# Kernel optimization log

Hardware: AMD Instinct MI355X
Metric: run time of the kernel (lower is better)

The kernel has to match this reference:

```python
import jax, jax.numpy as jnp
import numpy as np

B, N = 2, 384
NODE_DIM, NODE_HIDDEN, EDGE_DIM = 128, 256, 64
EDGE_H1 = 2 * EDGE_DIM + 2 * NODE_DIM  # 384, forced by concat in edge update
EDGE_H2 = 128
HEADS = 8
SCALE = 1.0 / float(np.sqrt(NODE_HIDDEN // HEADS))  # torch uses node_hidden//heads
EPS = 1e-5


def _w(k, out_dim, in_dim):
    return jax.random.normal(k, (out_dim, in_dim), dtype=jnp.float32) * 0.02


def setup_inputs() -> dict:
    ks = jax.random.split(jax.random.key(0), 32)
    inp = {
        'x': jax.random.normal(ks[0], (B, N, NODE_DIM), dtype=jnp.float32),
        'dense_adj': jax.random.normal(ks[1], (B, N, N, EDGE_DIM), dtype=jnp.float32),
        'wnq': _w(ks[2], NODE_DIM, NODE_DIM),
        'wnk': _w(ks[3], NODE_DIM, NODE_DIM),
        'wnv': _w(ks[4], NODE_DIM, NODE_DIM),
        'weq': _w(ks[5], NODE_DIM, EDGE_DIM),
        'wek': _w(ks[6], NODE_DIM, EDGE_DIM),
        'wev': _w(ks[7], NODE_DIM, EDGE_DIM),
        'nfc1_w': _w(ks[8], NODE_DIM, NODE_DIM),
        'nfc1_b': jnp.zeros((NODE_DIM,), jnp.float32),
        'ln1_g': jnp.ones((NODE_DIM,), jnp.float32),
        'ln1_b': jnp.zeros((NODE_DIM,), jnp.float32),
        'nfc2_w': _w(ks[9], NODE_HIDDEN, NODE_DIM),
        'nfc2_b': jnp.zeros((NODE_HIDDEN,), jnp.float32),
        'nfc3_w': _w(ks[10], NODE_DIM, NODE_HIDDEN),
        'nfc3_b': jnp.zeros((NODE_DIM,), jnp.float32),
        'ln2_g': jnp.ones((NODE_DIM,), jnp.float32),
        'ln2_b': jnp.zeros((NODE_DIM,), jnp.float32),
        'efc1_w': _w(ks[11], EDGE_DIM, EDGE_H1),
        'efc1_b': jnp.zeros((EDGE_DIM,), jnp.float32),
        'efc2_w': _w(ks[12], EDGE_DIM, EDGE_DIM),
        'efc2_b': jnp.zeros((EDGE_DIM,), jnp.float32),
        'eln1_g': jnp.ones((EDGE_DIM,), jnp.float32),
        'eln1_b': jnp.zeros((EDGE_DIM,), jnp.float32),
        'efc3_w': _w(ks[13], EDGE_H2, EDGE_DIM),
        'efc3_b': jnp.zeros((EDGE_H2,), jnp.float32),
        'efc4_w': _w(ks[14], EDGE_DIM, EDGE_H2),
        'efc4_b': jnp.zeros((EDGE_DIM,), jnp.float32),
        'eln2_g': jnp.ones((EDGE_DIM,), jnp.float32),
        'eln2_b': jnp.zeros((EDGE_DIM,), jnp.float32),
    }
    return inp


def layer_norm(t, g, b):
    m = jnp.mean(t, axis=-1, keepdims=True)
    v = jnp.mean((t - m) ** 2, axis=-1, keepdims=True)
    return (t - m) * jax.lax.rsqrt(v + EPS) * g + b


def rt_attention(x, adj, wnq, wnk, wnv, weq, wek, wev):
    Bb, Nn, D = x.shape
    d = D // HEADS
    def sn(t):  # [B,N,D] -> [B,H,N,d]
        return t.reshape(Bb, Nn, HEADS, d).transpose(0, 2, 1, 3)
    def se(t):  # [B,N,N,D] -> [B,H,N,N,d]
        return t.reshape(Bb, Nn, Nn, HEADS, d).transpose(0, 3, 1, 2, 4)
    # edge-augmented per-pair q,k,v: [B,H,i,j,d]
    q = sn(x @ wnq.T)[:, :, :, None, :] + se(adj @ weq.T)
    k = sn(x @ wnk.T)[:, :, None, :, :] + se(adj @ wek.T)
    v = sn(x @ wnv.T)[:, :, None, :, :] + se(adj @ wev.T)
    scores = jnp.sum(q * k, axis=-1) * SCALE          # [B,H,i,j]
    attn = jax.nn.softmax(scores, axis=-1)            # softmax over keys j
    out = jnp.einsum('bhij,bhijc->bhic', attn, v)     # [B,H,N,d]
    # torch reshape_from_batches interleaves as [B,N,d,H] -> [B,N,d*H]
    return out.transpose(0, 2, 3, 1).reshape(Bb, Nn, D)


def reference(x, dense_adj, wnq, wnk, wnv, weq, wek, wev,
              nfc1_w, nfc1_b, ln1_g, ln1_b, nfc2_w, nfc2_b, nfc3_w, nfc3_b,
              ln2_g, ln2_b, efc1_w, efc1_b, efc2_w, efc2_b, eln1_g, eln1_b,
              efc3_w, efc3_b, efc4_w, efc4_b, eln2_g, eln2_b):
    attn_out = rt_attention(x, dense_adj, wnq, wnk, wnv, weq, wek, wev)
    res = attn_out @ nfc1_w.T + nfc1_b
    x = layer_norm(x + res, ln1_g, ln1_b)
    res = jax.nn.relu(x @ nfc2_w.T + nfc2_b) @ nfc3_w.T + nfc3_b
    x = layer_norm(x + res, ln2_g, ln2_b)
    # edge update: [adj_ij, adj_ji, x_j (source), x_i (target)]
    Bb, Nn, D = x.shape
    src = jnp.broadcast_to(x[:, None, :, :], (Bb, Nn, Nn, D))
    tgt = jnp.broadcast_to(x[:, :, None, :], (Bb, Nn, Nn, D))
    rev = jnp.swapaxes(dense_adj, -2, -3)
    ua = jnp.concatenate([dense_adj, rev, src, tgt], axis=-1)  # [B,N,N,EDGE_H1]
    res = jax.nn.relu(ua @ efc1_w.T + efc1_b) @ efc2_w.T + efc2_b
    adj = layer_norm(dense_adj + res, eln1_g, eln1_b)
    res = jax.nn.relu(adj @ efc3_w.T + efc3_b) @ efc4_w.T + efc4_b
    adj = layer_norm(adj + res, eln2_g, eln2_b)
    return (x, adj)
```

## Files before the change

### kernel.cpp

```cpp
#include <hip/hip_runtime.h>
#include <hip/hip_bf16.h>

typedef unsigned short u16;
typedef unsigned int u32;

#define NB 2
#define NN 384
#define ND 128
#define NE 64
#define NHD 8
#define NHID 256
#define EH1 384
#define EH2 128
#define LN_EPS 1e-5f
#define ATT_SCALE 0.17677669529663687f

#define XOUT_ELEMS (NB * NN * ND)
#define ADJ_ELEMS ((size_t)NB * NN * NN * NE)
#define OUT_ELEMS (XOUT_ELEMS + ADJ_ELEMS)
#define SCRATCH_F32 (4 * XOUT_ELEMS)

typedef __attribute__((ext_vector_type(4))) float f32x4;
typedef __attribute__((ext_vector_type(8))) short s16x8;
#define MFMA16(a, b, c) __builtin_amdgcn_mfma_f32_16x16x32_bf16(a, b, c, 0, 0, 0)

__device__ __forceinline__ float bflo(u32 u) {
  return __builtin_bit_cast(float, u << 16);
}
__device__ __forceinline__ float bfhi(u32 u) {
  return __builtin_bit_cast(float, u & 0xffff0000u);
}
__device__ __forceinline__ u16 bfr(float f) {
  return __builtin_bit_cast(u16, __float2bfloat16(f));
}
__device__ __forceinline__ float bfu(u16 h) {
  return __builtin_bit_cast(float, ((u32)h) << 16);
}
__device__ __forceinline__ u32 packbf(float a, float b) {
  return (u32)bfr(a) | ((u32)bfr(b) << 16);
}
__device__ __forceinline__ float wsum64(float v) {
#pragma unroll
  for (int o = 32; o > 0; o >>= 1) v += __shfl_xor(v, o, 64);
  return v;
}
__device__ __forceinline__ float wmax64(float v) {
#pragma unroll
  for (int o = 32; o > 0; o >>= 1) v = fmaxf(v, __shfl_xor(v, o, 64));
  return v;
}

__device__ __forceinline__ s16x8 cvt_frag(const float* p) {
  float4 a = *(const float4*)p;
  float4 c = *(const float4*)(p + 4);
  s16x8 r;
  r[0] = (short)bfr(a.x); r[1] = (short)bfr(a.y);
  r[2] = (short)bfr(a.z); r[3] = (short)bfr(a.w);
  r[4] = (short)bfr(c.x); r[5] = (short)bfr(c.y);
  r[6] = (short)bfr(c.z); r[7] = (short)bfr(c.w);
  return r;
}

__device__ __forceinline__ void cvt8_hl(const float* p, uint4& hi, uint4& lo) {
  float4 a = *(const float4*)p;
  float4 c = *(const float4*)(p + 4);
  float v[8] = {a.x, a.y, a.z, a.w, c.x, c.y, c.z, c.w};
  u32 hw[4], lw[4];
#pragma unroll
  for (int e = 0; e < 4; ++e) {
    u16 h0 = bfr(v[2 * e]), h1 = bfr(v[2 * e + 1]);
    u16 l0 = bfr(v[2 * e] - bfu(h0));
    u16 l1 = bfr(v[2 * e + 1] - bfu(h1));
    hw[e] = (u32)h0 | ((u32)h1 << 16);
    lw[e] = (u32)l0 | ((u32)l1 << 16);
  }
  hi.x = hw[0]; hi.y = hw[1]; hi.z = hw[2]; hi.w = hw[3];
  lo.x = lw[0]; lo.y = lw[1]; lo.z = lw[2]; lo.w = lw[3];
}

__global__ void k_node_qkv(const float* __restrict__ x,
                           const float* __restrict__ wq,
                           const float* __restrict__ wk,
                           const float* __restrict__ wv,
                           float* __restrict__ nq, float* __restrict__ nk,
                           float* __restrict__ nv) {
  int row = blockIdx.x;
  int t = threadIdx.x;
  __shared__ float xs[ND];
  xs[t] = x[row * ND + t];
  __syncthreads();
  float aq = 0.f, ak = 0.f, av = 0.f;
  for (int k = 0; k < ND; ++k) {
    float xv = xs[k];
    aq += xv * wq[t * ND + k];
    ak += xv * wk[t * ND + k];
    av += xv * wv[t * ND + k];
  }
  nq[row * ND + t] = aq;
  nk[row * ND + t] = ak;
  nv[row * ND + t] = av;
}

#define ATJ 128
struct AttnS {
  u16 Ahi[ATJ][NE];
  u16 Alo[ATJ][NE];
  float sc[NHD][NN];
  float psum[NHD][NE];
  float part[4][ND];
};

__global__ void __launch_bounds__(512) k_attn(
    const float* __restrict__ adj,
    const float* __restrict__ weq,
    const float* __restrict__ wek,
    const float* __restrict__ wev,
    const float* __restrict__ nq,
    const float* __restrict__ nk,
    const float* __restrict__ nv,
    float* __restrict__ att) {
  __shared__ AttnS s;
  int bi = blockIdx.x;
  int b = bi / NN;
  int t = threadIdx.x;
  int h = t >> 6;
  int l = t & 63;
  int lr = l & 15, lk = l >> 4;

  s16x8 BQ[2], BK[2];
  {
    const float* wqp = weq + (size_t)(h * 16 + lr) * NE + lk * 8;
    const float* wkp = wek + (size_t)(h * 16 + lr) * NE + lk * 8;
    BQ[0] = cvt_frag(wqp); BQ[1] = cvt_frag(wqp + 32);
    BK[0] = cvt_frag(wkp); BK[1] = cvt_frag(wkp + 32);
  }
  float nqd = nq[(size_t)bi * ND + h * 16 + lr];

  for (int tile = 0; tile < NN / ATJ; ++tile) {
    int jbase = tile * ATJ;
    __syncthreads();
    for (int p = t; p < ATJ * 8; p += 512) {
      int row = p >> 3, u = p & 7;
      const float* src = adj + ((size_t)bi * NN + jbase + row) * NE + u * 8;
      uint4 hi, lo;
      cvt8_hl(src, hi, lo);
      int byt = (row * 128 + u * 16) ^ ((row & 7) << 4);
      *(uint4*)((char*)s.Ahi + byt) = hi;
      *(uint4*)((char*)s.Alo + byt) = lo;
    }
    __syncthreads();

#pragma unroll
    for (int sub = 0; sub < ATJ / 16; ++sub) {
      int trow = sub * 16 + lr;
      int swz = (trow & 7) << 4;
      f32x4 eq = {0.f, 0.f, 0.f, 0.f}, ek = {0.f, 0.f, 0.f, 0.f};
#pragma unroll
      for (int ks = 0; ks < 2; ++ks) {
        int byt = (trow * 128 + ks * 64 + lk * 16) ^ swz;
        s16x8 ah = *(const s16x8*)((const char*)s.Ahi + byt);
        s16x8 al = *(const s16x8*)((const char*)s.Alo + byt);
        eq = MFMA16(ah, BQ[ks], eq);
        eq = MFMA16(al, BQ[ks], eq);
        ek = MFMA16(ah, BK[ks], ek);
        ek = MFMA16(al, BK[ks], ek);
      }
#pragma unroll
      for (int r = 0; r < 4; ++r) {
        int j = jbase + sub * 16 + lk * 4 + r;
        float kv = nk[((size_t)b * NN + j) * ND + h * 16 + lr] + ek[r];
        float prod = (nqd + eq[r]) * kv;
#pragma unroll
        for (int o = 8; o > 0; o >>= 1) prod += __shfl_xor(prod, o, 64);
        if (lr == 0) s.sc[h][j] = prod * ATT_SCALE;
      }
    }
  }
  __syncthreads();

  {
    float vals[NN / 64];
    float m = -1e30f;
#pragma unroll
    for (int r = 0; r < NN / 64; ++r) {
      vals[r] = s.sc[h][l + 64 * r];
      m = fmaxf(m, vals[r]);
    }
    m = wmax64(m);
    float sum = 0.f;
#pragma unroll
    for (int r = 0; r < NN / 64; ++r) {
      vals[r] = __expf(vals[r] - m);
      sum += vals[r];
    }
    sum = wsum64(sum);
    float rinv = 1.f / sum;
#pragma unroll
    for (int r = 0; r < NN / 64; ++r) s.sc[h][l + 64 * r] = vals[r] * rinv;
  }

  {
    float pacc = 0.f;
    const float* ab = adj + (size_t)bi * NN * NE + l;
    const float* prow = s.sc[h];
#pragma unroll 4
    for (int j = 0; j < NN; ++j) pacc += prow[j] * ab[(size_t)j * NE];
    s.psum[h][l] = pacc;
  }
  __syncthreads();

  {
    int c = t & 127, grp = t >> 7;
    int hc = c >> 4;
    float acc = 0.f;
    const float* nvb = nv + (size_t)b * NN * ND + c;
    const float* pr = s.sc[hc];
#pragma unroll 4
    for (int j = grp * (NN / 4); j < (grp + 1) * (NN / 4); ++j)
      acc += pr[j] * nvb[(size_t)j * ND];
    s.part[grp][c] = acc;
  }
  __syncthreads();
  if (t < ND) {
    int c = t, hc = c >> 4;
    float acc = s.part[0][c] + s.part[1][c] + s.part[2][c] + s.part[3][c];
    const float4* wr = (const float4*)(wev + c * NE);
    const float* ps = s.psum[hc];
#pragma unroll
    for (int k4 = 0; k4 < NE / 4; ++k4) {
      float4 w4 = wr[k4];
      acc += w4.x * ps[4 * k4] + w4.y * ps[4 * k4 + 1] +
             w4.z * ps[4 * k4 + 2] + w4.w * ps[4 * k4 + 3];
    }
    att[(size_t)bi * ND + (c & 15) * NHD + hc] = acc;
  }
}

struct FfnS {
  float atts[ND];
  float tvb[ND];
  float x1[ND];
  float hb[NHID];
  float stats[2];
};

__global__ void k_node_ffn(const float* __restrict__ x,
                           const float* __restrict__ att,
                           const float* __restrict__ w1, const float* __restrict__ b1,
                           const float* __restrict__ g1, const float* __restrict__ bb1,
                           const float* __restrict__ w2, const float* __restrict__ b2,
                           const float* __restrict__ w3, const float* __restrict__ b3,
                           const float* __restrict__ g2, const float* __restrict__ bb2,
                           float* __restrict__ xout) {
  __shared__ FfnS s;
  int row = blockIdx.x;
  int tid = threadIdx.x;
  if (tid < ND) s.atts[tid] = att[row * ND + tid];
  __syncthreads();

  if (tid < ND) {
    float acc = b1[tid];
    for (int k = 0; k < ND; ++k) acc += s.atts[k] * w1[tid * ND + k];
    s.tvb[tid] = x[row * ND + tid] + acc;
  }
  __syncthreads();
  if (tid < 64) {
    float v0 = s.tvb[tid], v1 = s.tvb[tid + 64];
    float m = wsum64(v0 + v1) * (1.f / ND);
    float d0 = v0 - m, d1 = v1 - m;
    float var = wsum64(d0 * d0 + d1 * d1) * (1.f / ND);
    if (tid == 0) {
      s.stats[0] = m;
      s.stats[1] = rsqrtf(var + LN_EPS);
    }
  }
  __syncthreads();
  if (tid < ND)
    s.x1[tid] = (s.tvb[tid] - s.stats[0]) * s.stats[1] * g1[tid] + bb1[tid];
  __syncthreads();

  {
    float acc = b2[tid];
    for (int k = 0; k < ND; ++k) acc += s.x1[k] * w2[tid * ND + k];
    s.hb[tid] = fmaxf(acc, 0.f);
  }
  __syncthreads();

  if (tid < ND) {
    float acc = b3[tid];
    for (int k = 0; k < NHID; ++k) acc += s.hb[k] * w3[tid * NHID + k];
    s.tvb[tid] = s.x1[tid] + acc;
  }
  __syncthreads();
  if (tid < 64) {
    float v0 = s.tvb[tid], v1 = s.tvb[tid + 64];
    float m = wsum64(v0 + v1) * (1.f / ND);
    float d0 = v0 - m, d1 = v1 - m;
    float var = wsum64(d0 * d0 + d1 * d1) * (1.f / ND);
    if (tid == 0) {
      s.stats[0] = m;
      s.stats[1] = rsqrtf(var + LN_EPS);
    }
  }
  __syncthreads();
  if (tid < ND) {
    float o = (s.tvb[tid] - s.stats[0]) * s.stats[1] * g2[tid] + bb2[tid];
    xout[row * ND + tid] = o;
  }
}

#define EMT 32

struct E1M {
  u16 Ahi[EMT][256];
  u16 Alo[EMT][256];
  u16 Hhi[EMT][NE];
  u16 Hlo[EMT][NE];
};

__global__ void __launch_bounds__(512) k_edge1(
    const float* __restrict__ adj, const float* __restrict__ xq,
    const float* __restrict__ w1, const float* __restrict__ b1,
    const float* __restrict__ w2, const float* __restrict__ b2,
    const float* __restrict__ g, const float* __restrict__ bb,
    float* __restrict__ adj1out) {
  __shared__ E1M s;
  int bi = blockIdx.x;
  int b = bi / NN, i = bi % NN;
  int t = threadIdx.x;
  int w = t >> 6, l = t & 63;
  int m16 = (w & 1) * 16;
  int n16 = (w >> 1) * 16;
  int lr = l & 15, lk = l >> 4;

  s16x8 B1[8], B2[2];
  {
    const float* wr = w1 + (size_t)(n16 + lr) * EH1 + lk * 8;
#pragma unroll
    for (int ks = 0; ks < 8; ++ks) B1[ks] = cvt_frag(wr + ks * 32);
    const float* w2r = w2 + (size_t)(n16 + lr) * NE + lk * 8;
#pragma unroll
    for (int ks = 0; ks < 2; ++ks) B2[ks] = cvt_frag(w2r + ks * 32);
  }
  float bias1;
  {
    float ci = 0.f;
    const float* xr = xq + (size_t)bi * ND;
    const float* wr = w1 + (size_t)(n16 + lr) * EH1 + 256;
#pragma unroll 4
    for (int k = 0; k < ND; ++k) ci += xr[k] * bfu(bfr(wr[k]));
    bias1 = b1[n16 + lr] + ci;
  }
  float bias2 = b2[n16 + lr];
  float gl = g[l], bl = bb[l];

  for (int mt = 0; mt < NN / EMT; ++mt) {
    int jbase = mt * EMT;
    __syncthreads();
    for (int p = t; p < EMT * 32; p += 512) {
      int row = p >> 5, uu = p & 31;
      const float* src;
      if (uu < 8)
        src = adj + ((size_t)bi * NN + jbase + row) * NE + uu * 8;
      else if (uu < 16)
        src = adj + ((size_t)(b * NN + jbase + row) * NN + i) * NE + (uu - 8) * 8;
      else
        src = xq + (size_t)(b * NN + jbase + row) * ND + (uu - 16) * 8;
      uint4 hi, lo;
      cvt8_hl(src, hi, lo);
      int byt = (row * 512 + uu * 16) ^ ((row & 7) << 4);
      *(uint4*)((char*)s.Ahi + byt) = hi;
      *(uint4*)((char*)s.Alo + byt) = lo;
    }
    __syncthreads();

    f32x4 acc = {0.f, 0.f, 0.f, 0.f};
    int arow = m16 + lr;
    int aswz = (arow & 7) << 4;
#pragma unroll
    for (int ks = 0; ks < 8; ++ks) {
      int byt = (arow * 512 + ks * 64 + lk * 16) ^ aswz;
      s16x8 ah = *(const s16x8*)((const char*)s.Ahi + byt);
      s16x8 al = *(const s16x8*)((const char*)s.Alo + byt);
      acc = MFMA16(ah, B1[ks], acc);
      acc = MFMA16(al, B1[ks], acc);
    }
#pragma unroll
    for (int r = 0; r < 4; ++r) {
      float hv = fmaxf(acc[r] + bias1, 0.f);
      u16 hh = bfr(hv);
      u16 hl = bfr(hv - bfu(hh));
      int row = m16 + lk * 4 + r;
      int byt = (row * 128 + (n16 + lr) * 2) ^ ((row & 7) << 4);
      *(u16*)((char*)s.Hhi + byt) = hh;
      *(u16*)((char*)s.Hlo + byt) = hl;
    }
    __syncthreads();

    f32x4 acc2 = {0.f, 0.f, 0.f, 0.f};
#pragma unroll
    for (int ks = 0; ks < 2; ++ks) {
      int byt = (arow * 128 + ks * 64 + lk * 16) ^ aswz;
      s16x8 ah = *(const s16x8*)((const char*)s.Hhi + byt);
      s16x8 al = *(const s16x8*)((const char*)s.Hlo + byt);
      acc2 = MFMA16(ah, B2[ks], acc2);
      acc2 = MFMA16(al, B2[ks], acc2);
    }
    __syncthreads();
    float* tvb = (float*)s.Hhi;
#pragma unroll
    for (int r = 0; r < 4; ++r) {
      int row = m16 + lk * 4 + r;
      int col = n16 + lr;
      int abyt = (row * 512 + col * 2) ^ ((row & 7) << 4);
      float aorig = bfu(*(const u16*)((const char*)s.Ahi + abyt)) +
                    bfu(*(const u16*)((const char*)s.Alo + abyt));
      tvb[row * NE + col] = aorig + acc2[r] + bias2;
    }
    __syncthreads();
#pragma unroll
    for (int rr = 0; rr < EMT / 8; ++rr) {
      int row = w * (EMT / 8) + rr;
      float tv = tvb[row * NE + l];
      float mean = wsum64(tv) * (1.f / NE);
      float dv = tv - mean;
      float var = wsum64(dv * dv) * (1.f / NE);
      float o = dv * rsqrtf(var + LN_EPS) * gl + bl;
      adj1out[((size_t)bi * NN + jbase + row) * NE + l] = o;
    }
  }
}

struct E2M {
  u16 Ahi[EMT][NE];
  u16 Alo[EMT][NE];
  u16 Hhi[EMT][EH2];
  u16 Hlo[EMT][EH2];
};

__global__ void __launch_bounds__(512) k_edge2(
    float* __restrict__ adjio,
    const float* __restrict__ w3, const float* __restrict__ b3,
    const float* __restrict__ w4, const float* __restrict__ b4,
    const float* __restrict__ g, const float* __restrict__ bb) {
  __shared__ E2M s;
  int bi = blockIdx.x;
  int t = threadIdx.x;
  int w = t >> 6, l = t & 63;
  int m16 = (w & 1) * 16;
  int nb = (w >> 1) * 2;
  int n16 = (w >> 1) * 16;
  int lr = l & 15, lk = l >> 4;

  s16x8 B3[2][2], B4[4];
  {
#pragma unroll
    for (int n = 0; n < 2; ++n) {
      const float* wr = w3 + (size_t)((nb + n) * 16 + lr) * NE + lk * 8;
#pragma unroll
      for (int ks = 0; ks < 2; ++ks) B3[n][ks] = cvt_frag(wr + ks * 32);
    }
    const float* w4r = w4 + (size_t)(n16 + lr) * EH2 + lk * 8;
#pragma unroll
    for (int ks = 0; ks < 4; ++ks) B4[ks] = cvt_frag(w4r + ks * 32);
  }
  float bias3[2] = {b3[nb * 16 + lr], b3[(nb + 1) * 16 + lr]};
  float bias4 = b4[n16 + lr];
  float gl = g[l], bl = bb[l];

  for (int mt = 0; mt < NN / EMT; ++mt) {
    int jbase = mt * EMT;
    __syncthreads();
    for (int p = t; p < EMT * 8; p += 512) {
      int row = p >> 3, u = p & 7;
      const float* src = adjio + ((size_t)bi * NN + jbase + row) * NE + u * 8;
      uint4 hi, lo;
      cvt8_hl(src, hi, lo);
      int byt = (row * 128 + u * 16) ^ ((row & 7) << 4);
      *(uint4*)((char*)s.Ahi + byt) = hi;
      *(uint4*)((char*)s.Alo + byt) = lo;
    }
    __syncthreads();

    f32x4 a3[2] = {{0.f, 0.f, 0.f, 0.f}, {0.f, 0.f, 0.f, 0.f}};
    int arow = m16 + lr;
    int aswz = (arow & 7) << 4;
#pragma unroll
    for (int ks = 0; ks < 2; ++ks) {
      int byt = (arow * 128 + ks * 64 + lk * 16) ^ aswz;
      s16x8 ah = *(const s16x8*)((const char*)s.Ahi + byt);
      s16x8 al = *(const s16x8*)((const char*)s.Alo + byt);
#pragma unroll
      for (int n = 0; n < 2; ++n) {
        a3[n] = MFMA16(ah, B3[n][ks], a3[n]);
        a3[n] = MFMA16(al, B3[n][ks], a3[n]);
      }
    }
#pragma unroll
    for (int n = 0; n < 2; ++n) {
#pragma unroll
      for (int r = 0; r < 4; ++r) {
        float hv = fmaxf(a3[n][r] + bias3[n], 0.f);
        u16 hh = bfr(hv);
        u16 hl = bfr(hv - bfu(hh));
        int row = m16 + lk * 4 + r;
        int byt = (row * 256 + ((nb + n) * 16 + lr) * 2) ^ ((row & 7) << 4);
        *(u16*)((char*)s.Hhi + byt) = hh;
        *(u16*)((char*)s.Hlo + byt) = hl;
      }
    }
    __syncthreads();

    f32x4 a4 = {0.f, 0.f, 0.f, 0.f};
#pragma unroll
    for (int ks = 0; ks < 4; ++ks) {
      int byt = (arow * 256 + ks * 64 + lk * 16) ^ aswz;
      s16x8 ah = *(const s16x8*)((const char*)s.Hhi + byt);
      s16x8 al = *(const s16x8*)((const char*)s.Hlo + byt);
      a4 = MFMA16(ah, B4[ks], a4);
      a4 = MFMA16(al, B4[ks], a4);
    }
    __syncthreads();
    float* tvb = (float*)s.Hhi;
#pragma unroll
    for (int r = 0; r < 4; ++r) {
      int row = m16 + lk * 4 + r;
      int col = n16 + lr;
      int abyt = (row * 128 + col * 2) ^ ((row & 7) << 4);
      float aorig = bfu(*(const u16*)((const char*)s.Ahi + abyt)) +
                    bfu(*(const u16*)((const char*)s.Alo + abyt));
      tvb[row * NE + col] = aorig + a4[r] + bias4;
    }
    __syncthreads();
#pragma unroll
    for (int rr = 0; rr < EMT / 8; ++rr) {
      int row = w * (EMT / 8) + rr;
      float tv = tvb[row * NE + l];
      float mean = wsum64(tv) * (1.f / NE);
      float dv = tv - mean;
      float var = wsum64(dv * dv) * (1.f / NE);
      float o = dv * rsqrtf(var + LN_EPS) * gl + bl;
      adjio[((size_t)bi * NN + jbase + row) * NE + l] = o;
    }
  }
}

extern "C" void kernel_launch(void* const* d_in, const int* in_sizes, int n_in,
                              void* d_out, int out_size, void* d_ws, size_t ws_size,
                              hipStream_t stream) {
  (void)in_sizes; (void)n_in; (void)out_size; (void)d_ws; (void)ws_size;
  const float* x      = (const float*)d_in[0];
  const float* adj    = (const float*)d_in[1];
  const float* wnq    = (const float*)d_in[2];
  const float* wnk    = (const float*)d_in[3];
  const float* wnv    = (const float*)d_in[4];
  const float* weq    = (const float*)d_in[5];
  const float* wek    = (const float*)d_in[6];
  const float* wev    = (const float*)d_in[7];
  const float* nfc1_w = (const float*)d_in[8];
  const float* nfc1_b = (const float*)d_in[9];
  const float* ln1_g  = (const float*)d_in[10];
  const float* ln1_b  = (const float*)d_in[11];
  const float* nfc2_w = (const float*)d_in[12];
  const float* nfc2_b = (const float*)d_in[13];
  const float* nfc3_w = (const float*)d_in[14];
  const float* nfc3_b = (const float*)d_in[15];
  const float* ln2_g  = (const float*)d_in[16];
  const float* ln2_b  = (const float*)d_in[17];
  const float* efc1_w = (const float*)d_in[18];
  const float* efc1_b = (const float*)d_in[19];
  const float* efc2_w = (const float*)d_in[20];
  const float* efc2_b = (const float*)d_in[21];
  const float* eln1_g = (const float*)d_in[22];
  const float* eln1_b = (const float*)d_in[23];
  const float* efc3_w = (const float*)d_in[24];
  const float* efc3_b = (const float*)d_in[25];
  const float* efc4_w = (const float*)d_in[26];
  const float* efc4_b = (const float*)d_in[27];
  const float* eln2_g = (const float*)d_in[28];
  const float* eln2_b = (const float*)d_in[29];

  float* outf = (float*)d_out;
  float* outadj = outf + XOUT_ELEMS;

  float* scratch = outf + OUT_ELEMS - SCRATCH_F32;
  float* nq  = scratch;
  float* nk  = scratch + XOUT_ELEMS;
  float* nv  = scratch + 2 * XOUT_ELEMS;
  float* att = scratch + 3 * XOUT_ELEMS;

  k_node_qkv<<<NB * NN, 128, 0, stream>>>(x, wnq, wnk, wnv, nq, nk, nv);
  k_attn<<<NB * NN, 512, 0, stream>>>(adj, weq, wek, wev, nq, nk, nv, att);
  k_node_ffn<<<NB * NN, 256, 0, stream>>>(x, att, nfc1_w, nfc1_b, ln1_g, ln1_b,
                                          nfc2_w, nfc2_b, nfc3_w, nfc3_b,
                                          ln2_g, ln2_b, outf);
  k_edge1<<<NB * NN, 512, 0, stream>>>(adj, outf, efc1_w, efc1_b, efc2_w, efc2_b,
                                       eln1_g, eln1_b, outadj);
  k_edge2<<<NB * NN, 512, 0, stream>>>(outadj, efc3_w, efc3_b, efc4_w, efc4_b,
                                       eln2_g, eln2_b);
}
```

Measured before the change: 570.3 us.

## Prefetch adj tiles into registers and fuse online softmax with edge-value accumulation

The attention kernel now loads the next adj tile into registers while the current tile is being processed, and preloads nk values for the whole tile into a register array. An online softmax (running max and sum) computes the probability-weighted sum of adj rows from the bf16 hi/lo tile already in shared memory, instead of rereading all of adj from global memory in a second pass. This removes a second pass over global memory and hides load latency, at the cost of more registers, extra shared memory for pe, and a small precision change from reconstructing adj from its hi/lo bf16 split.

```diff
diff --git a/kernel.cpp b/kernel.cpp
--- a/kernel.cpp
+++ b/kernel.cpp
@@ -61,9 +61,7 @@
   return r;
 }
 
-__device__ __forceinline__ void cvt8_hl(const float* p, uint4& hi, uint4& lo) {
-  float4 a = *(const float4*)p;
-  float4 c = *(const float4*)(p + 4);
+__device__ __forceinline__ void cvt8v(float4 a, float4 c, uint4& hi, uint4& lo) {
   float v[8] = {a.x, a.y, a.z, a.w, c.x, c.y, c.z, c.w};
   u32 hw[4], lw[4];
 #pragma unroll
@@ -76,6 +74,10 @@
   }
   hi.x = hw[0]; hi.y = hw[1]; hi.z = hw[2]; hi.w = hw[3];
   lo.x = lw[0]; lo.y = lw[1]; lo.z = lw[2]; lo.w = lw[3];
+}
+
+__device__ __forceinline__ void cvt8_hl(const float* p, uint4& hi, uint4& lo) {
+  cvt8v(*(const float4*)p, *(const float4*)(p + 4), hi, lo);
 }
 
 __global__ void k_node_qkv(const float* __restrict__ x,
@@ -106,6 +108,7 @@
   u16 Ahi[ATJ][NE];
   u16 Alo[ATJ][NE];
   float sc[NHD][NN];
+  float pe[NHD][ATJ];
   float psum[NHD][NE];
   float part[4][ND];
 };
@@ -136,19 +139,52 @@
   }
   float nqd = nq[(size_t)bi * ND + h * 16 + lr];
 
+  int row0 = t >> 3, u0 = t & 7;
+  int row1 = row0 + 64, u1 = u0;
+  float4 pa0, pb0, pa1, pb1;
+  {
+    const float* s0 = adj + ((size_t)bi * NN + row0) * NE + u0 * 8;
+    const float* s1 = adj + ((size_t)bi * NN + row1) * NE + u1 * 8;
+    pa0 = *(const float4*)s0; pb0 = *(const float4*)(s0 + 4);
+    pa1 = *(const float4*)s1; pb1 = *(const float4*)(s1 + 4);
+  }
+
+  float m_run = -1e30f, lsum = 0.f, psacc = 0.f;
+
   for (int tile = 0; tile < NN / ATJ; ++tile) {
     int jbase = tile * ATJ;
     __syncthreads();
-    for (int p = t; p < ATJ * 8; p += 512) {
-      int row = p >> 3, u = p & 7;
-      const float* src = adj + ((size_t)bi * NN + jbase + row) * NE + u * 8;
+    {
       uint4 hi, lo;
-      cvt8_hl(src, hi, lo);
-      int byt = (row * 128 + u * 16) ^ ((row & 7) << 4);
+      cvt8v(pa0, pb0, hi, lo);
+      int byt = (row0 * 128 + u0 * 16) ^ ((row0 & 7) << 4);
       *(uint4*)((char*)s.Ahi + byt) = hi;
       *(uint4*)((char*)s.Alo + byt) = lo;
-    }
-    __syncthreads();
+      cvt8v(pa1, pb1, hi, lo);
+      byt = (row1 * 128 + u1 * 16) ^ ((row1 & 7) << 4);
+      *(uint4*)((char*)s.Ahi + byt) = hi;
+      *(uint4*)((char*)s.Alo + byt) = lo;
+    }
+    __syncthreads();
+
+    {
+      int tn = (tile < NN / ATJ - 1) ? tile + 1 : 0;
+      const float* s0 = adj + ((size_t)bi * NN + tn * ATJ + row0) * NE + u0 * 8;
+      const float* s1 = adj + ((size_t)bi * NN + tn * ATJ + row1) * NE + u1 * 8;
+      pa0 = *(const float4*)s0; pb0 = *(const float4*)(s0 + 4);
+      pa1 = *(const float4*)s1; pb1 = *(const float4*)(s1 + 4);
+    }
+
+    float nkv[32];
+    {
+      const float* nkb =
+          nk + ((size_t)b * NN + jbase + lk * 4) * ND + h * 16 + lr;
+#pragma unroll
+      for (int sub = 0; sub < 8; ++sub)
+#pragma unroll
+        for (int r = 0; r < 4; ++r)
+          nkv[sub * 4 + r] = nkb[(size_t)(sub * 16 + r) * ND];
+    }
 
 #pragma unroll
     for (int sub = 0; sub < ATJ / 16; ++sub) {
@@ -168,44 +204,47 @@
 #pragma unroll
       for (int r = 0; r < 4; ++r) {
         int j = jbase + sub * 16 + lk * 4 + r;
-        float kv = nk[((size_t)b * NN + j) * ND + h * 16 + lr] + ek[r];
+        float kv = nkv[sub * 4 + r] + ek[r];
         float prod = (nqd + eq[r]) * kv;
 #pragma unroll
         for (int o = 8; o > 0; o >>= 1) prod += __shfl_xor(prod, o, 64);
         if (lr == 0) s.sc[h][j] = prod * ATT_SCALE;
       }
     }
-  }
-  __syncthreads();
-
-  {
-    float vals[NN / 64];
-    float m = -1e30f;
+    __builtin_amdgcn_wave_barrier();
+
+    {
+      float s0v = s.sc[h][jbase + l];
+      float s1v = s.sc[h][jbase + 64 + l];
+      float tmax = wmax64(fmaxf(s0v, s1v));
+      float m_new = fmaxf(m_run, tmax);
+      float f = __expf(m_run - m_new);
+      float e0 = __expf(s0v - m_new), e1 = __expf(s1v - m_new);
+      s.pe[h][l] = e0;
+      s.pe[h][l + 64] = e1;
+      lsum = lsum * f + wsum64(e0 + e1);
+      psacc *= f;
+      m_run = m_new;
+      __builtin_amdgcn_wave_barrier();
+#pragma unroll 8
+      for (int j = 0; j < ATJ; ++j) {
+        float pj = s.pe[h][j];
+        int byt = (j * 128 + l * 2) ^ ((j & 7) << 4);
+        float av = bfu(*(const u16*)((const char*)s.Ahi + byt)) +
+                   bfu(*(const u16*)((const char*)s.Alo + byt));
+        psacc += pj * av;
+      }
+    }
+  }
+
+  {
+    float rinv = 1.f / lsum;
 #pragma unroll
     for (int r = 0; r < NN / 64; ++r) {
-      vals[r] = s.sc[h][l + 64 * r];
-      m = fmaxf(m, vals[r]);
-    }
-    m = wmax64(m);
-    float sum = 0.f;
-#pragma unroll
-    for (int r = 0; r < NN / 64; ++r) {
-      vals[r] = __expf(vals[r] - m);
-      sum += vals[r];
-    }
-    sum = wsum64(sum);
-    float rinv = 1.f / sum;
-#pragma unroll
-    for (int r = 0; r < NN / 64; ++r) s.sc[h][l + 64 * r] = vals[r] * rinv;
-  }
-
-  {
-    float pacc = 0.f;
-    const float* ab = adj + (size_t)bi * NN * NE + l;
-    const float* prow = s.sc[h];
-#pragma unroll 4
-    for (int j = 0; j < NN; ++j) pacc += prow[j] * ab[(size_t)j * NE];
-    s.psum[h][l] = pacc;
+      float sv = s.sc[h][l + 64 * r];
+      s.sc[h][l + 64 * r] = __expf(sv - m_run) * rinv;
+    }
+    s.psum[h][l] = psacc * rinv;
   }
   __syncthreads();
 
```

Result: no change. 563.8 us (-1.1%).
